# Kernel optimization log

Measured on AMD Instinct MI355X. Metric: run time of the kernel, lower is better.

## Reference

```python
import jax, jax.numpy as jnp
import numpy as np

B, N, H, T = 64, 64, 128, 128


def setup_inputs() -> dict:
    key = jax.random.key(0)
    ks = jax.random.split(key, 8)
    tf = jax.random.normal(ks[0], (B, N, H, T), dtype=jnp.float32)
    # learnable symmetric adjacency parameter
    ap = jax.random.normal(ks[1], (N, N), dtype=jnp.float32) * 0.1
    ap = (ap + ap.T) / 2
    # edge MLP params (stored as (in, out) for x @ W)
    W1 = jax.random.normal(ks[2], (2 * H, H), dtype=jnp.float32) * (1.0 / np.sqrt(2 * H))
    b1 = jnp.zeros((H,), dtype=jnp.float32)
    W2 = jax.random.normal(ks[3], (H, H // 2), dtype=jnp.float32) * (1.0 / np.sqrt(H))
    b2 = jnp.zeros((H // 2,), dtype=jnp.float32)
    W3 = jax.random.normal(ks[4], (H // 2, 1), dtype=jnp.float32) * (1.0 / np.sqrt(H // 2))
    b3 = jnp.zeros((1,), dtype=jnp.float32)
    return {"temporal_features": tf, "adj_param": ap, "W1": W1, "b1": b1,
            "W2": W2, "b2": b2, "W3": W3, "b3": b3}


def reference(temporal_features, adj_param, W1, b1, W2, b2, W3, b3):
    # node features: mean over time -> (B, N, H)
    node = temporal_features.mean(axis=-1)
    h_dim = node.shape[-1]
    # concat([h_i, h_j]) @ W1 == h_i @ W1[:H] + h_j @ W1[H:]  (avoids materializing 2H concat)
    Wi, Wj = W1[:h_dim], W1[h_dim:]
    pi = jnp.einsum('bnh,hk->bnk', node, Wi)  # (B, N, H)
    pj = jnp.einsum('bnh,hk->bnk', node, Wj)
    h = jax.nn.relu(pi[:, :, None, :] + pj[:, None, :, :] + b1)  # (B, N, N, H)
    # Dropout(0.2) is identity at inference
    h = jax.nn.relu(jnp.einsum('bijh,hk->bijk', h, W2) + b2)      # (B, N, N, H//2)
    feat_adj = (jnp.einsum('bijk,ko->bijo', h, W3) + b3)[..., 0]  # (B, N, N)
    # combined method
    adj = 0.5 * adj_param[None, :, :] + 0.5 * feat_adj
    # symmetrize + relu
    adj = jax.nn.relu((adj + jnp.swapaxes(adj, -2, -1)) / 2)
    # add self-loops and degree-normalize rows
    adj = adj + jnp.eye(adj.shape[-1], dtype=adj.dtype)[None]
    adj = adj / (adj.sum(axis=-1, keepdims=True) + 1e-8)
    return adj
```

## Files before the change

kernel.cpp:

```cpp
#include <hip/hip_runtime.h>
#include <stdint.h>
#include <stddef.h>

typedef __attribute__((ext_vector_type(8))) short short8;
typedef __attribute__((ext_vector_type(4))) float f32x4;
typedef __attribute__((ext_vector_type(4))) unsigned uint4v;

__device__ inline unsigned short f2bf(float x) {
    unsigned u = __float_as_uint(x);
    unsigned r = (u + 0x7fffu + ((u >> 16) & 1u)) >> 16;
    return (unsigned short)r;
}

__device__ inline unsigned pk2t(float lo, float hi) {
    return __builtin_amdgcn_perm(__float_as_uint(hi), __float_as_uint(lo), 0x07060302u);
}

template <int CTRL>
__device__ inline float dpp_add(float v) {
    int t = __builtin_amdgcn_update_dpp(0, __float_as_int(v), CTRL, 0xF, 0xF, true);
    return v + __int_as_float(t);
}
__device__ inline float row16_sum(float v) {
    v = dpp_add<0xB1>(v);
    v = dpp_add<0x4E>(v);
    v = dpp_add<0x124>(v);
    v = dpp_add<0x128>(v);
    return v;
}

__global__ __launch_bounds__(256) void k1_mean(const float* __restrict__ tf,
                                               const float* __restrict__ W1,
                                               float* __restrict__ node,
                                               unsigned short* __restrict__ w1t_g) {
    if (blockIdx.x < 64) {
        int base = blockIdx.x * 512 + threadIdx.x * 2;
#pragma unroll
        for (int e = 0; e < 2; ++e) {
            int idx = base + e;
            int c = idx >> 7, k = idx & 127;
            int ch = c >> 7, n = c & 127;
            w1t_g[idx] = f2bf(W1[(size_t)ch * 16384 + (size_t)k * 128 + n]);
        }
    }
    int wave = (blockIdx.x * blockDim.x + threadIdx.x) >> 6;
    int lane = threadIdx.x & 63;
    int half = lane >> 5;
    int c = lane & 31;
    const f32x4* tf4 = reinterpret_cast<const f32x4*>(tf);
    size_t base = (size_t)wave * 8 * 64;

    f32x4 v[8];
#pragma unroll
    for (int k = 0; k < 8; ++k) v[k] = __builtin_nontemporal_load(&tf4[base + (size_t)k * 64 + lane]);

    float s[8];
#pragma unroll
    for (int k = 0; k < 8; ++k) s[k] = (v[k][0] + v[k][1]) + (v[k][2] + v[k][3]);
#pragma unroll
    for (int m = 1; m <= 16; m <<= 1) {
#pragma unroll
        for (int k = 0; k < 8; ++k) s[k] += __shfl_xor(s[k], m);
    }
    if (c == 0) {
#pragma unroll
        for (int k = 0; k < 8; ++k) {
            int rp = wave * 8 + k;
            node[(size_t)rp * 2 + half] = s[k] * (1.0f / 128.0f);
        }
    }
}

__global__ __launch_bounds__(512) void k2_proj(const float* __restrict__ node,
                                               const unsigned short* __restrict__ w1t_g,
                                               const float* __restrict__ b1,
                                               const float* __restrict__ W2,
                                               float* __restrict__ pi,
                                               float* __restrict__ pj,
                                               unsigned short* __restrict__ w2t_g) {
    const int LP = 136;
    __shared__ unsigned short A_lds[16 * LP];
    __shared__ unsigned short BT[128 * LP];
    __shared__ float b1s[128];

    int tid = threadIdx.x;
    int rblk = blockIdx.x >> 1;
    int half = blockIdx.x & 1;
    int r0 = rblk * 16;

    if (blockIdx.x < 16) {
        int idx = blockIdx.x * 512 + tid;
        int m = idx >> 7, k = idx & 127;
        w2t_g[idx] = f2bf(W2[(size_t)k * 64 + m]);
    }

    {
        int row = tid >> 5;
        int c0 = (tid & 31) * 4;
        float4 v = *reinterpret_cast<const float4*>(node + (size_t)(r0 + row) * 128 + c0);
        unsigned wb[2];
        wb[0] = (unsigned)f2bf(v.x) | ((unsigned)f2bf(v.y) << 16);
        wb[1] = (unsigned)f2bf(v.z) | ((unsigned)f2bf(v.w) << 16);
        *reinterpret_cast<uint2*>(&A_lds[row * LP + c0]) = *reinterpret_cast<uint2*>(wb);
    }
    {
        int n = tid >> 2;
        int q = tid & 3;
        const uint4v* src = reinterpret_cast<const uint4v*>(w1t_g + ((size_t)(half * 128 + n) * 128 + q * 32));
        uint4v* dst = reinterpret_cast<uint4v*>(&BT[n * LP + q * 32]);
#pragma unroll
        for (int e = 0; e < 4; ++e) dst[e] = src[e];
    }
    if (tid < 128) b1s[tid] = b1[tid];
    __syncthreads();

    int w = tid >> 6;
    int l = tid & 63;
    int lr = l & 15;
    int lg = l >> 4;

    f32x4 acc = {0, 0, 0, 0};
#pragma unroll
    for (int ks = 0; ks < 4; ++ks) {
        int kb = ks * 32 + lg * 8;
        short8 afrag = *reinterpret_cast<const short8*>(&A_lds[lr * LP + kb]);
        short8 bfrag = *reinterpret_cast<const short8*>(&BT[(w * 16 + lr) * LP + kb]);
        acc = __builtin_amdgcn_mfma_f32_16x16x32_bf16(afrag, bfrag, acc, 0, 0, 0);
    }
    float* out = half ? pj : pi;
    int col = w * 16 + lr;
    float bias = half ? 0.0f : b1s[col];
#pragma unroll
    for (int r = 0; r < 4; ++r) {
        int row = r0 + lg * 4 + r;
        out[(size_t)row * 128 + col] = acc[r] + bias;
    }
}

__global__ __launch_bounds__(256) void k3_mlp(const float* __restrict__ pi,
                                              const float* __restrict__ pj,
                                              const unsigned short* __restrict__ w2t_g,
                                              const float* __restrict__ b2,
                                              const float* __restrict__ W3,
                                              const float* __restrict__ b3,
                                              float* __restrict__ F) {
    const int LDA = 136;
    __shared__ unsigned short W2T[64 * LDA];
    __shared__ float pipb8[8][128];
    __shared__ float b2s[64], w3s[64];

    int tid = threadIdx.x;
    int b = blockIdx.x >> 3;
    int it = blockIdx.x & 7;
    int i0 = it * 8;

    int w = tid >> 6;
    int l = tid & 63;
    int lr = l & 15;
    int lg = l >> 4;

    float pjreg[32];
    {
        const float* pjrow = pj + (size_t)(b * 64 + w * 16 + lr) * 128;
#pragma unroll
        for (int ks = 0; ks < 4; ++ks) {
            float4 q0 = *reinterpret_cast<const float4*>(pjrow + ks * 32 + lg * 8);
            float4 q1 = *reinterpret_cast<const float4*>(pjrow + ks * 32 + lg * 8 + 4);
            pjreg[ks * 8 + 0] = q0.x; pjreg[ks * 8 + 1] = q0.y;
            pjreg[ks * 8 + 2] = q0.z; pjreg[ks * 8 + 3] = q0.w;
            pjreg[ks * 8 + 4] = q1.x; pjreg[ks * 8 + 5] = q1.y;
            pjreg[ks * 8 + 6] = q1.z; pjreg[ks * 8 + 7] = q1.w;
        }
    }
    {
        int row = tid >> 5;
        int c4 = tid & 31;
        float4 v = reinterpret_cast<const float4*>(pi + ((size_t)(b * 64 + i0 + row) * 128))[c4];
        reinterpret_cast<float4*>(&pipb8[row][0])[c4] = v;
    }
    {
        int m = tid >> 2;
        int q = tid & 3;
        const uint4v* src = reinterpret_cast<const uint4v*>(w2t_g + (size_t)m * 128 + q * 32);
        uint4v* dst = reinterpret_cast<uint4v*>(&W2T[m * LDA + q * 32]);
#pragma unroll
        for (int e = 0; e < 4; ++e) dst[e] = src[e];
    }
    if (tid < 64) {
        b2s[tid] = b2[tid];
        w3s[tid] = W3[tid];
    }
    float b3v = b3[0];
    __syncthreads();

    short8 bfr[4][4];
#pragma unroll
    for (int ks = 0; ks < 4; ++ks) {
        int kb = ks * 32 + lg * 8;
#pragma unroll
        for (int nt = 0; nt < 4; ++nt)
            bfr[ks][nt] = *reinterpret_cast<const short8*>(&W2T[(nt * 16 + lr) * LDA + kb]);
    }

#pragma unroll 2
    for (int il = 0; il < 8; ++il) {
        f32x4 acc0 = {0.f, 0.f, 0.f, 0.f};
        f32x4 acc1 = {0.f, 0.f, 0.f, 0.f};
        f32x4 acc2 = {0.f, 0.f, 0.f, 0.f};
        f32x4 acc3 = {0.f, 0.f, 0.f, 0.f};
        const float4* prow = reinterpret_cast<const float4*>(&pipb8[il][0]);
#pragma unroll
        for (int ks = 0; ks < 4; ++ks) {
            float4 pa = prow[ks * 8 + lg * 2];
            float4 pb = prow[ks * 8 + lg * 2 + 1];
            unsigned au[4];
            au[0] = pk2t(fmaxf(pa.x + pjreg[ks * 8 + 0], 0.0f),
                         fmaxf(pa.y + pjreg[ks * 8 + 1], 0.0f));
            au[1] = pk2t(fmaxf(pa.z + pjreg[ks * 8 + 2], 0.0f),
                         fmaxf(pa.w + pjreg[ks * 8 + 3], 0.0f));
            au[2] = pk2t(fmaxf(pb.x + pjreg[ks * 8 + 4], 0.0f),
                         fmaxf(pb.y + pjreg[ks * 8 + 5], 0.0f));
            au[3] = pk2t(fmaxf(pb.z + pjreg[ks * 8 + 6], 0.0f),
                         fmaxf(pb.w + pjreg[ks * 8 + 7], 0.0f));
            short8 afrag = *reinterpret_cast<short8*>(au);
            acc0 = __builtin_amdgcn_mfma_f32_16x16x32_bf16(afrag, bfr[ks][0], acc0, 0, 0, 0);
            acc1 = __builtin_amdgcn_mfma_f32_16x16x32_bf16(afrag, bfr[ks][1], acc1, 0, 0, 0);
            acc2 = __builtin_amdgcn_mfma_f32_16x16x32_bf16(afrag, bfr[ks][2], acc2, 0, 0, 0);
            acc3 = __builtin_amdgcn_mfma_f32_16x16x32_bf16(afrag, bfr[ks][3], acc3, 0, 0, 0);
        }
        float part[4] = {0.f, 0.f, 0.f, 0.f};
#pragma unroll
        for (int mt = 0; mt < 4; ++mt) {
            int m = mt * 16 + lr;
            float w3 = w3s[m];
            float bb = b2s[m];
            f32x4 a = (mt == 0) ? acc0 : (mt == 1) ? acc1 : (mt == 2) ? acc2 : acc3;
#pragma unroll
            for (int r = 0; r < 4; ++r) {
                float h = fmaxf(a[r] + bb, 0.0f);
                part[r] += h * w3;
            }
        }
#pragma unroll
        for (int r = 0; r < 4; ++r) part[r] = row16_sum(part[r]);
        if (lr == 0) {
#pragma unroll
            for (int r = 0; r < 4; ++r) {
                int j = w * 16 + lg * 4 + r;
                F[((size_t)b * 64 + i0 + il) * 64 + j] = part[r] + b3v;
            }
        }
    }
}

__global__ __launch_bounds__(512) void k4_final(const float* __restrict__ F,
                                                const float* __restrict__ ap,
                                                float* __restrict__ out) {
    __shared__ float s[64][65];
    int b = blockIdx.x >> 1;
    int rh = (blockIdx.x & 1) * 32;
    int tid = threadIdx.x;
    for (int idx = tid; idx < 4096; idx += 512) {
        s[idx >> 6][idx & 63] = F[(size_t)b * 4096 + idx];
    }
    __syncthreads();
    int wv = tid >> 6, lane = tid & 63;
#pragma unroll
    for (int itr = 0; itr < 4; ++itr) {
        int i = rh + wv * 4 + itr;
        float a_ij = ap[i * 64 + lane];
        float v = 0.5f * a_ij + 0.25f * (s[i][lane] + s[lane][i]);
        v = fmaxf(v, 0.0f);
        if (i == lane) v += 1.0f;
        float sum = v;
        sum += __shfl_xor(sum, 1);
        sum += __shfl_xor(sum, 2);
        sum += __shfl_xor(sum, 4);
        sum += __shfl_xor(sum, 8);
        sum += __shfl_xor(sum, 16);
        sum += __shfl_xor(sum, 32);
        out[(size_t)b * 4096 + i * 64 + lane] = v / (sum + 1e-8f);
    }
}

extern "C" void kernel_launch(void* const* d_in, const int* in_sizes, int n_in,
                              void* d_out, int out_size, void* d_ws, size_t ws_size,
                              hipStream_t stream) {
    const float* tf = (const float*)d_in[0];
    const float* ap = (const float*)d_in[1];
    const float* W1 = (const float*)d_in[2];
    const float* b1 = (const float*)d_in[3];
    const float* W2 = (const float*)d_in[4];
    const float* b2 = (const float*)d_in[5];
    const float* W3 = (const float*)d_in[6];
    const float* b3 = (const float*)d_in[7];
    float* out = (float*)d_out;

    char* ws = (char*)d_ws;
    float* node = (float*)(ws);
    float* pi   = (float*)(ws + (size_t)(2 << 20));
    float* pj   = (float*)(ws + (size_t)(4 << 20));
    float* F    = (float*)(ws + (size_t)(6 << 20));
    unsigned short* w2t_g = (unsigned short*)(ws + (size_t)(7 << 20));
    unsigned short* w1t_g = (unsigned short*)(ws + (size_t)(7 << 20) + 65536);

    k1_mean<<<8192, 256, 0, stream>>>(tf, W1, node, w1t_g);
    k2_proj<<<512, 512, 0, stream>>>(node, w1t_g, b1, W2, pi, pj, w2t_g);
    k3_mlp<<<512, 256, 0, stream>>>(pi, pj, w2t_g, b2, W3, b3, F);
    k4_final<<<128, 512, 0, stream>>>(F, ap, out);
}
```

Measured before the change: 65.66 us.

## Fuse final normalization into MLP kernel via last-block atomic counter

Removes the separate k4_final launch by having each MLP block increment a per-batch atomic counter after writing its F tile. The eighth (last) block for a batch reloads the full 64x64 F slice and performs symmetrization, relu, self-loop and row normalization. The counters are reset inside k2_proj. This saves one kernel launch and its gap, at the cost of fences, an atomic per block, and a serialized tail done by only 64 blocks with 256 threads each.

```diff
diff --git a/kernel.cpp b/kernel.cpp
--- a/kernel.cpp
+++ b/kernel.cpp
@@ -77,7 +77,8 @@
                                                const float* __restrict__ W2,
                                                float* __restrict__ pi,
                                                float* __restrict__ pj,
-                                               unsigned short* __restrict__ w2t_g) {
+                                               unsigned short* __restrict__ w2t_g,
+                                               unsigned* __restrict__ cnt) {
     const int LP = 136;
     __shared__ unsigned short A_lds[16 * LP];
     __shared__ unsigned short BT[128 * LP];
@@ -93,6 +94,7 @@
         int m = idx >> 7, k = idx & 127;
         w2t_g[idx] = f2bf(W2[(size_t)k * 64 + m]);
     }
+    if (blockIdx.x == 100 && tid < 64) cnt[tid] = 0;
 
     {
         int row = tid >> 5;
@@ -137,17 +139,22 @@
     }
 }
 
-__global__ __launch_bounds__(256) void k3_mlp(const float* __restrict__ pi,
-                                              const float* __restrict__ pj,
-                                              const unsigned short* __restrict__ w2t_g,
-                                              const float* __restrict__ b2,
-                                              const float* __restrict__ W3,
-                                              const float* __restrict__ b3,
-                                              float* __restrict__ F) {
+__global__ __launch_bounds__(256) void k34_mlp(const float* __restrict__ pi,
+                                               const float* __restrict__ pj,
+                                               const unsigned short* __restrict__ w2t_g,
+                                               const float* __restrict__ b2,
+                                               const float* __restrict__ W3,
+                                               const float* __restrict__ b3,
+                                               const float* __restrict__ ap,
+                                               float* __restrict__ F,
+                                               float* __restrict__ outp,
+                                               unsigned* __restrict__ cnt) {
     const int LDA = 136;
     __shared__ unsigned short W2T[64 * LDA];
     __shared__ float pipb8[8][128];
     __shared__ float b2s[64], w3s[64];
+    __shared__ float s[64][65];
+    __shared__ int amLast;
 
     int tid = threadIdx.x;
     int b = blockIdx.x >> 3;
@@ -251,35 +258,37 @@
             }
         }
     }
-}
-
-__global__ __launch_bounds__(512) void k4_final(const float* __restrict__ F,
-                                                const float* __restrict__ ap,
-                                                float* __restrict__ out) {
-    __shared__ float s[64][65];
-    int b = blockIdx.x >> 1;
-    int rh = (blockIdx.x & 1) * 32;
-    int tid = threadIdx.x;
-    for (int idx = tid; idx < 4096; idx += 512) {
-        s[idx >> 6][idx & 63] = F[(size_t)b * 4096 + idx];
-    }
+
+    __threadfence();
     __syncthreads();
-    int wv = tid >> 6, lane = tid & 63;
-#pragma unroll
-    for (int itr = 0; itr < 4; ++itr) {
-        int i = rh + wv * 4 + itr;
-        float a_ij = ap[i * 64 + lane];
-        float v = 0.5f * a_ij + 0.25f * (s[i][lane] + s[lane][i]);
-        v = fmaxf(v, 0.0f);
-        if (i == lane) v += 1.0f;
-        float sum = v;
-        sum += __shfl_xor(sum, 1);
-        sum += __shfl_xor(sum, 2);
-        sum += __shfl_xor(sum, 4);
-        sum += __shfl_xor(sum, 8);
-        sum += __shfl_xor(sum, 16);
-        sum += __shfl_xor(sum, 32);
-        out[(size_t)b * 4096 + i * 64 + lane] = v / (sum + 1e-8f);
+    if (tid == 0) {
+        unsigned prev = atomicAdd(&cnt[b], 1u);
+        amLast = (prev == 7u);
+    }
+    __syncthreads();
+    if (amLast) {
+        __threadfence();
+        for (int idx = tid; idx < 4096; idx += 256) {
+            s[idx >> 6][idx & 63] = F[(size_t)b * 4096 + idx];
+        }
+        __syncthreads();
+        int lane = l;
+#pragma unroll
+        for (int itr = 0; itr < 16; ++itr) {
+            int i = w + 4 * itr;
+            float a_ij = ap[i * 64 + lane];
+            float v = 0.5f * a_ij + 0.25f * (s[i][lane] + s[lane][i]);
+            v = fmaxf(v, 0.0f);
+            if (i == lane) v += 1.0f;
+            float sum = v;
+            sum += __shfl_xor(sum, 1);
+            sum += __shfl_xor(sum, 2);
+            sum += __shfl_xor(sum, 4);
+            sum += __shfl_xor(sum, 8);
+            sum += __shfl_xor(sum, 16);
+            sum += __shfl_xor(sum, 32);
+            outp[(size_t)b * 4096 + i * 64 + lane] = v / (sum + 1e-8f);
+        }
     }
 }
 
@@ -303,9 +312,9 @@
     float* F    = (float*)(ws + (size_t)(6 << 20));
     unsigned short* w2t_g = (unsigned short*)(ws + (size_t)(7 << 20));
     unsigned short* w1t_g = (unsigned short*)(ws + (size_t)(7 << 20) + 65536);
+    unsigned* cnt = (unsigned*)(ws + (size_t)(7 << 20) + 131072);
 
     k1_mean<<<8192, 256, 0, stream>>>(tf, W1, node, w1t_g);
-    k2_proj<<<512, 512, 0, stream>>>(node, w1t_g, b1, W2, pi, pj, w2t_g);
-    k3_mlp<<<512, 256, 0, stream>>>(pi, pj, w2t_g, b2, W3, b3, F);
-    k4_final<<<128, 512, 0, stream>>>(F, ap, out);
-}
+    k2_proj<<<512, 512, 0, stream>>>(node, w1t_g, b1, W2, pi, pj, w2t_g, cnt);
+    k34_mlp<<<512, 256, 0, stream>>>(pi, pj, w2t_g, b2, W3, b3, ap, F, out, cnt);
+}
```

Result: slower. 118.6 us (+80.6%).
